# Kernel optimization log

Measured on AMD Instinct MI355X. Metric: run time of the kernel, lower is better.

Reference implementation:

```python
import jax, jax.numpy as jnp
import numpy as np

B, T, D_MODEL, NHEAD, D_HEAD = 8, 4096, 1024, 16, 64


def setup_inputs() -> dict:
    key = jax.random.key(0)
    ks = jax.random.split(key, 8)
    return {
        "inputs": jax.random.normal(ks[0], (B, T, D_MODEL), jnp.float32),
        "z0": jax.random.normal(ks[1], (NHEAD, D_HEAD), jnp.float32),
        "W_in": jax.random.normal(ks[2], (D_MODEL, D_MODEL), jnp.float32) / np.sqrt(D_MODEL),
        "b_in": jax.random.normal(ks[3], (D_MODEL,), jnp.float32) * 0.01,
        "W_out": jax.random.normal(ks[4], (D_MODEL, D_MODEL), jnp.float32) / np.sqrt(D_MODEL),
        "b_out": jax.random.normal(ks[5], (D_MODEL,), jnp.float32) * 0.01,
        "smoothing_logit": jax.random.normal(ks[6], (NHEAD, 1), jnp.float32),
        "v0": jax.random.normal(ks[7], (1, 1, NHEAD, D_HEAD), jnp.float32),
    }


def reference(inputs, z0, W_in, b_in, W_out, b_out, smoothing_logit, v0):
    b, t, d = inputs.shape
    nhead, d_head = z0.shape
    # in projection -> (b, t, h, d_head)
    values = (inputs @ W_in + b_in).reshape(b, t, nhead, d_head)
    # prepend learned z0, then temporal differencing -> (b, t, h, d_head)
    z0_b = jnp.broadcast_to(z0[None, None], (b, 1, nhead, d_head))
    values = jnp.concatenate([z0_b, values], axis=1)
    values = values[:, 1:] - values[:, :-1]
    # exponential smoothing recurrence: s_j = a*s_{j-1} + (1-a)*v_j, s_{-1} = v0
    alpha = jax.nn.sigmoid(smoothing_logit)           # (h, 1)
    a = alpha[None]                                   # (1, h, 1) broadcast over batch
    s0 = jnp.broadcast_to(v0[0, 0][None], (b, nhead, d_head))

    def step(s, v):                                   # v: (b, h, d_head)
        s = a * s + (1.0 - a) * v
        return s, s

    _, es_out = jax.lax.scan(step, s0, jnp.swapaxes(values, 0, 1))  # (t, b, h, d)
    es_out = jnp.swapaxes(es_out, 0, 1)               # (b, t, h, d_head)
    # prepend v0 -> length t+1
    v0_b = jnp.broadcast_to(v0, (b, 1, nhead, d_head))
    out = jnp.concatenate([v0_b, es_out], axis=1)     # (b, t+1, h, d_head)
    out = out.reshape(b, t + 1, nhead * d_head)
    return out @ W_out + b_out                        # (b, t+1, d_model)
```

## Files before the change

kernel.cpp:

```cpp
#include <hip/hip_runtime.h>
#include <hip/hip_bf16.h>
#include <stdint.h>

#define DEV static __device__ __forceinline__

typedef __attribute__((ext_vector_type(8))) short bf16x8;
typedef __attribute__((ext_vector_type(4))) float f32x4;
typedef unsigned int u32;

static constexpr int T = 4096;
static constexpr int BATCH = 8;
static constexpr int DM = 1024;
static constexpr int M1 = BATCH * T;
static constexpr int M2 = BATCH * (T + 1);
static constexpr int M2P = 257 * 128;
static constexpr int NCH = 64;
static constexpr int CL = T / NCH;
static constexpr int NT = 16;

DEV unsigned short f2bf(float f) {
  union { float f; unsigned u; } v; v.f = f;
  unsigned u = v.u;
  return (unsigned short)((u + 0x7fffu + ((u >> 16) & 1u)) >> 16);
}
DEV float bf2f(unsigned short s) {
  union { unsigned u; float f; } v; v.u = ((unsigned)s) << 16;
  return v.f;
}

DEV void gl_lds16(const unsigned short* g, unsigned short* lds) {
  __builtin_amdgcn_global_load_lds(
      (const __attribute__((address_space(1))) u32*)g,
      (__attribute__((address_space(3))) u32*)lds,
      16, 0, 0);
}

__global__ void k_cvt_x(const float4* __restrict__ x, ushort4* __restrict__ o) {
  int i = blockIdx.x * 256 + threadIdx.x;
  float4 v = x[i];
  ushort4 r;
  r.x = f2bf(v.x); r.y = f2bf(v.y); r.z = f2bf(v.z); r.w = f2bf(v.w);
  o[i] = r;
}

__global__ void k_transpose(const float* __restrict__ w0, const float* __restrict__ w1,
                            unsigned short* __restrict__ t0, unsigned short* __restrict__ t1) {
  __shared__ float tile[32][33];
  const float* src = blockIdx.z ? w1 : w0;
  unsigned short* dst = blockIdx.z ? t1 : t0;
  int bx = blockIdx.x * 32;
  int by = blockIdx.y * 32;
  int tx = threadIdx.x & 31, ty = threadIdx.x >> 5;
#pragma unroll
  for (int r = 0; r < 32; r += 8)
    tile[ty + r][tx] = src[(by + ty + r) * DM + bx + tx];
  __syncthreads();
#pragma unroll
  for (int r = 0; r < 32; r += 8)
    dst[(bx + ty + r) * DM + by + tx] = f2bf(tile[tx][ty + r]);
}

template <int MODE>
__global__ __launch_bounds__(256, 2) void k_gemm(const unsigned short* __restrict__ A16,
                                                 const unsigned short* __restrict__ Bt16,
                                                 const float* __restrict__ bias,
                                                 unsigned short* __restrict__ outb,
                                                 float* __restrict__ outf, int Mvalid) {
  __shared__ unsigned short lds[2][2][128 * 64];

  const int tid = threadIdx.x;
  const int w = tid >> 6, l = tid & 63;
  const int wm = w >> 1, wn = w & 1;
  const int lo = l & 15, hi = l >> 4;

  const int nwg = gridDim.x, orig = blockIdx.x;
  const int cpx = nwg >> 3;
  const int wg = (orig & 7) * cpx + (orig >> 3);
  const int bm = wg >> 3, bn = wg & 7;
  const int blockM = bm * 128;
  const int blockN = bn * 128;

  f32x4 acc[4][4];
#pragma unroll
  for (int m = 0; m < 4; m++)
#pragma unroll
    for (int n = 0; n < 4; n++) acc[m][n] = (f32x4){0.f, 0.f, 0.f, 0.f};

  const int ssw = (l & 7) ^ ((l >> 3) & 7);
  const unsigned short* pA[4];
  const unsigned short* pB[4];
#pragma unroll
  for (int c = 0; c < 4; c++) {
    const int rp = w * 32 + c * 8 + (l >> 3);
    pA[c] = A16 + (size_t)(blockM + rp) * DM + ssw * 8;
    pB[c] = Bt16 + (size_t)(blockN + rp) * DM + ssw * 8;
  }

  auto stage = [&](int tt, int buf) {
#pragma unroll
    for (int c = 0; c < 4; c++) {
      gl_lds16(pA[c] + (size_t)tt * 64, &lds[buf][0][(w * 32 + c * 8) * 64]);
      gl_lds16(pB[c] + (size_t)tt * 64, &lds[buf][1][(w * 32 + c * 8) * 64]);
    }
  };

  stage(0, 0);
  __syncthreads();

  for (int t = 0; t < NT; ++t) {
    const int cur = t & 1;
    if (t + 1 < NT) stage(t + 1, cur ^ 1);

    const unsigned short* La = lds[cur][0];
    const unsigned short* Lb = lds[cur][1];
    bf16x8 aq[4][2], bq[4][2];
#pragma unroll
    for (int kh = 0; kh < 2; kh++) {
      const int g = kh * 4 + hi;
#pragma unroll
      for (int mf = 0; mf < 4; mf++) {
        const int r = wm * 64 + mf * 16 + lo;
        aq[mf][kh] = *(const bf16x8*)(La + r * 64 + (g ^ (r & 7)) * 8);
      }
#pragma unroll
      for (int nf = 0; nf < 4; nf++) {
        const int r = wn * 64 + nf * 16 + lo;
        bq[nf][kh] = *(const bf16x8*)(Lb + r * 64 + (g ^ (r & 7)) * 8);
      }
    }
#pragma unroll
    for (int kh = 0; kh < 2; kh++)
#pragma unroll
      for (int mf = 0; mf < 4; mf++)
#pragma unroll
        for (int nf = 0; nf < 4; nf++)
          acc[mf][nf] = __builtin_amdgcn_mfma_f32_16x16x32_bf16(
              bq[nf][kh], aq[mf][kh], acc[mf][nf], 0, 0, 0);

    __syncthreads();
  }

#pragma unroll
  for (int mf = 0; mf < 4; mf++) {
    const int row = blockM + wm * 64 + mf * 16 + lo;
    if (MODE == 1 && row >= Mvalid) continue;
#pragma unroll
    for (int nf = 0; nf < 4; nf++) {
      const int col = blockN + wn * 64 + nf * 16 + hi * 4;
      const float4 bv = *(const float4*)(bias + col);
      if (MODE == 0) {
        ushort4 o;
        o.x = f2bf(acc[mf][nf][0] + bv.x);
        o.y = f2bf(acc[mf][nf][1] + bv.y);
        o.z = f2bf(acc[mf][nf][2] + bv.z);
        o.w = f2bf(acc[mf][nf][3] + bv.w);
        *(ushort4*)(outb + (size_t)row * DM + col) = o;
      } else {
        float4 o;
        o.x = acc[mf][nf][0] + bv.x;
        o.y = acc[mf][nf][1] + bv.y;
        o.z = acc[mf][nf][2] + bv.z;
        o.w = acc[mf][nf][3] + bv.w;
        *(float4*)(outf + (size_t)row * DM + col) = o;
      }
    }
  }
}

__global__ void k_scan_partial(const unsigned short* __restrict__ proj,
                               const float* __restrict__ logit,
                               const float* __restrict__ z0,
                               float* __restrict__ chunkend) {
  int b = blockIdx.x >> 6, c = blockIdx.x & 63;
  int ch = threadIdx.x;
  float a = 1.f / (1.f + expf(-logit[ch >> 6]));
  int t0 = c * CL;
  const unsigned short* p = proj + (size_t)(b * T + t0) * DM + ch;
  float pprev = (t0 == 0) ? z0[ch] : bf2f(p[-DM]);
  float s = 0.f;
  for (int j = 0; j < CL; j++) {
    float pv = bf2f(p[(size_t)j * DM]);
    s = a * s + (1.f - a) * (pv - pprev);
    pprev = pv;
  }
  chunkend[(b * NCH + c) * DM + ch] = s;
}

__global__ void k_scan_combine(const float* __restrict__ chunkend,
                               const float* __restrict__ logit,
                               const float* __restrict__ v0,
                               float* __restrict__ enter) {
  int b = blockIdx.x;
  int ch = threadIdx.x;
  float a = 1.f / (1.f + expf(-logit[ch >> 6]));
  float a2 = a * a, a4 = a2 * a2, a8 = a4 * a4, a16 = a8 * a8, a32 = a16 * a16;
  float aL = a32 * a32;
  float e = v0[ch];
  enter[(b * NCH + 0) * DM + ch] = e;
  for (int c = 1; c < NCH; c++) {
    e = aL * e + chunkend[(b * NCH + c - 1) * DM + ch];
    enter[(b * NCH + c) * DM + ch] = e;
  }
}

__global__ void k_scan_final(const unsigned short* __restrict__ proj,
                             const float* __restrict__ logit,
                             const float* __restrict__ z0,
                             const float* __restrict__ v0,
                             const float* __restrict__ enter,
                             unsigned short* __restrict__ S) {
  int b = blockIdx.x >> 6, c = blockIdx.x & 63;
  int ch = threadIdx.x;
  float a = 1.f / (1.f + expf(-logit[ch >> 6]));
  int t0 = c * CL;
  const unsigned short* p = proj + (size_t)(b * T + t0) * DM + ch;
  unsigned short* so = S + (size_t)(b * (T + 1) + t0 + 1) * DM + ch;
  float pprev = (t0 == 0) ? z0[ch] : bf2f(p[-DM]);
  float s = enter[(b * NCH + c) * DM + ch];
  if (c == 0) S[(size_t)b * (T + 1) * DM + ch] = f2bf(v0[ch]);
  for (int j = 0; j < CL; j++) {
    float pv = bf2f(p[(size_t)j * DM]);
    s = a * s + (1.f - a) * (pv - pprev);
    pprev = pv;
    so[(size_t)j * DM] = f2bf(s);
  }
}

__global__ void k_pad(unsigned short* __restrict__ S) {
  int i = blockIdx.x * 256 + threadIdx.x;
  S[(size_t)M2 * DM + i] = 0;
}

extern "C" void kernel_launch(void* const* d_in, const int* in_sizes, int n_in,
                              void* d_out, int out_size, void* d_ws, size_t ws_size,
                              hipStream_t stream) {
  const float* inputs = (const float*)d_in[0];
  const float* z0     = (const float*)d_in[1];
  const float* W_in   = (const float*)d_in[2];
  const float* b_in   = (const float*)d_in[3];
  const float* W_out  = (const float*)d_in[4];
  const float* b_out  = (const float*)d_in[5];
  const float* slogit = (const float*)d_in[6];
  const float* v0     = (const float*)d_in[7];
  float* out = (float*)d_out;

  char* ws = (char*)d_ws;
  unsigned short* X16   = (unsigned short*)(ws);
  unsigned short* P16   = (unsigned short*)(ws + 67108864);
  unsigned short* S16   = (unsigned short*)(ws + 134217728);
  unsigned short* WTin  = (unsigned short*)(ws + 201588736);
  unsigned short* WTout = (unsigned short*)(ws + 203685888);
  float* chunkend       = (float*)(ws + 205783040);
  float* enter          = (float*)(ws + 207880192);

  k_cvt_x<<<32768, 256, 0, stream>>>((const float4*)inputs, (ushort4*)X16);
  k_transpose<<<dim3(32, 32, 2), 256, 0, stream>>>(W_in, W_out, WTin, WTout);
  k_gemm<0><<<dim3((M1 / 128) * 8), 256, 0, stream>>>(X16, WTin, b_in, P16, nullptr, M1);
  k_scan_partial<<<dim3(BATCH * NCH), 1024, 0, stream>>>(P16, slogit, z0, chunkend);
  k_scan_combine<<<dim3(BATCH), 1024, 0, stream>>>(chunkend, slogit, v0, enter);
  k_scan_final<<<dim3(BATCH * NCH), 1024, 0, stream>>>(P16, slogit, z0, v0, enter, S16);
  k_pad<<<dim3(480), 256, 0, stream>>>(S16);
  k_gemm<1><<<dim3((M2P / 128) * 8), 256, 0, stream>>>(S16, WTout, b_out, nullptr, out, M2);
}
```

Before: 278.9 us.

## Fuse fp32-to-bf16 input conversion into first GEMM A-tile loading

Removes the standalone conversion kernel. The first GEMM now reads the fp32 inputs directly into registers, packs them to bf16 and writes them into swizzled LDS after the MFMA work, prefetching one k-tile ahead. This avoids writing and re-reading a bf16 copy of the activations. The zero-padding kernel for the second GEMM's pad rows is also dropped, since those rows are masked on store. In exchange, GEMM0 moves twice the A bytes through vector registers rather than async global-to-LDS loads, which adds register pressure and may reduce latency hiding.

```diff
diff --git a/kernel.cpp b/kernel.cpp
--- a/kernel.cpp
+++ b/kernel.cpp
@@ -27,20 +27,20 @@
   union { unsigned u; float f; } v; v.u = ((unsigned)s) << 16;
   return v.f;
 }
+DEV bf16x8 pack8(float4 a, float4 b) {
+  bf16x8 r;
+  r[0] = (short)f2bf(a.x); r[1] = (short)f2bf(a.y);
+  r[2] = (short)f2bf(a.z); r[3] = (short)f2bf(a.w);
+  r[4] = (short)f2bf(b.x); r[5] = (short)f2bf(b.y);
+  r[6] = (short)f2bf(b.z); r[7] = (short)f2bf(b.w);
+  return r;
+}
 
 DEV void gl_lds16(const unsigned short* g, unsigned short* lds) {
   __builtin_amdgcn_global_load_lds(
       (const __attribute__((address_space(1))) u32*)g,
       (__attribute__((address_space(3))) u32*)lds,
       16, 0, 0);
-}
-
-__global__ void k_cvt_x(const float4* __restrict__ x, ushort4* __restrict__ o) {
-  int i = blockIdx.x * 256 + threadIdx.x;
-  float4 v = x[i];
-  ushort4 r;
-  r.x = f2bf(v.x); r.y = f2bf(v.y); r.z = f2bf(v.z); r.w = f2bf(v.w);
-  o[i] = r;
 }
 
 __global__ void k_transpose(const float* __restrict__ w0, const float* __restrict__ w1,
@@ -61,7 +61,7 @@
 }
 
 template <int MODE>
-__global__ __launch_bounds__(256, 2) void k_gemm(const unsigned short* __restrict__ A16,
+__global__ __launch_bounds__(256, 2) void k_gemm(const void* __restrict__ Asrc,
                                                  const unsigned short* __restrict__ Bt16,
                                                  const float* __restrict__ bias,
                                                  unsigned short* __restrict__ outb,
@@ -80,6 +80,9 @@
   const int blockM = bm * 128;
   const int blockN = bn * 128;
 
+  const float* A32 = (const float*)Asrc;
+  const unsigned short* A16 = (const unsigned short*)Asrc;
+
   f32x4 acc[4][4];
 #pragma unroll
   for (int m = 0; m < 4; m++)
@@ -87,29 +90,60 @@
     for (int n = 0; n < 4; n++) acc[m][n] = (f32x4){0.f, 0.f, 0.f, 0.f};
 
   const int ssw = (l & 7) ^ ((l >> 3) & 7);
-  const unsigned short* pA[4];
   const unsigned short* pB[4];
+  const unsigned short* pA16[4];
 #pragma unroll
   for (int c = 0; c < 4; c++) {
     const int rp = w * 32 + c * 8 + (l >> 3);
-    pA[c] = A16 + (size_t)(blockM + rp) * DM + ssw * 8;
     pB[c] = Bt16 + (size_t)(blockN + rp) * DM + ssw * 8;
-  }
-
-  auto stage = [&](int tt, int buf) {
-#pragma unroll
-    for (int c = 0; c < 4; c++) {
-      gl_lds16(pA[c] + (size_t)tt * 64, &lds[buf][0][(w * 32 + c * 8) * 64]);
+    if (MODE == 1) pA16[c] = A16 + (size_t)(blockM + rp) * DM + ssw * 8;
+  }
+  auto stageB = [&](int tt, int buf) {
+#pragma unroll
+    for (int c = 0; c < 4; c++)
       gl_lds16(pB[c] + (size_t)tt * 64, &lds[buf][1][(w * 32 + c * 8) * 64]);
-    }
-  };
-
-  stage(0, 0);
+  };
+  auto stageA16 = [&](int tt, int buf) {
+#pragma unroll
+    for (int c = 0; c < 4; c++)
+      gl_lds16(pA16[c] + (size_t)tt * 64, &lds[buf][0][(w * 32 + c * 8) * 64]);
+  };
+
+  const int arow = tid >> 1;
+  const int akh = tid & 1;
+  const float* pA32 = A32 + (size_t)(blockM + arow) * DM + akh * 32;
+  float4 av[8];
+  auto loadA32 = [&](int tt) {
+#pragma unroll
+    for (int i = 0; i < 8; i++)
+      av[i] = *(const float4*)(pA32 + (size_t)tt * 64 + i * 4);
+  };
+  auto writeA32 = [&](int buf) {
+#pragma unroll
+    for (int s2 = 0; s2 < 4; s2++) {
+      const int s = akh * 4 + s2;
+      const int phys = s ^ (arow & 7);
+      *(bf16x8*)&lds[buf][0][arow * 64 + phys * 8] = pack8(av[s2 * 2], av[s2 * 2 + 1]);
+    }
+  };
+
+  if (MODE == 0) {
+    loadA32(0);
+    writeA32(0);
+  } else {
+    stageA16(0, 0);
+  }
+  stageB(0, 0);
   __syncthreads();
 
   for (int t = 0; t < NT; ++t) {
     const int cur = t & 1;
-    if (t + 1 < NT) stage(t + 1, cur ^ 1);
+    const bool hasN = (t + 1 < NT);
+    if (hasN) {
+      if (MODE == 0) loadA32(t + 1);
+      else           stageA16(t + 1, cur ^ 1);
+      stageB(t + 1, cur ^ 1);
+    }
 
     const unsigned short* La = lds[cur][0];
     const unsigned short* Lb = lds[cur][1];
@@ -136,6 +170,8 @@
         for (int nf = 0; nf < 4; nf++)
           acc[mf][nf] = __builtin_amdgcn_mfma_f32_16x16x32_bf16(
               bq[nf][kh], aq[mf][kh], acc[mf][nf], 0, 0, 0);
+
+    if (MODE == 0 && hasN) writeA32(cur ^ 1);
 
     __syncthreads();
   }
@@ -226,11 +262,6 @@
   }
 }
 
-__global__ void k_pad(unsigned short* __restrict__ S) {
-  int i = blockIdx.x * 256 + threadIdx.x;
-  S[(size_t)M2 * DM + i] = 0;
-}
-
 extern "C" void kernel_launch(void* const* d_in, const int* in_sizes, int n_in,
                               void* d_out, int out_size, void* d_ws, size_t ws_size,
                               hipStream_t stream) {
@@ -245,20 +276,17 @@
   float* out = (float*)d_out;
 
   char* ws = (char*)d_ws;
-  unsigned short* X16   = (unsigned short*)(ws);
-  unsigned short* P16   = (unsigned short*)(ws + 67108864);
-  unsigned short* S16   = (unsigned short*)(ws + 134217728);
-  unsigned short* WTin  = (unsigned short*)(ws + 201588736);
-  unsigned short* WTout = (unsigned short*)(ws + 203685888);
-  float* chunkend       = (float*)(ws + 205783040);
-  float* enter          = (float*)(ws + 207880192);
-
-  k_cvt_x<<<32768, 256, 0, stream>>>((const float4*)inputs, (ushort4*)X16);
+  unsigned short* P16   = (unsigned short*)(ws);
+  unsigned short* S16   = (unsigned short*)(ws + 67108864);
+  unsigned short* WTin  = (unsigned short*)(ws + 134479872);
+  unsigned short* WTout = (unsigned short*)(ws + 136577024);
+  float* chunkend       = (float*)(ws + 138674176);
+  float* enter          = (float*)(ws + 140771328);
+
   k_transpose<<<dim3(32, 32, 2), 256, 0, stream>>>(W_in, W_out, WTin, WTout);
-  k_gemm<0><<<dim3((M1 / 128) * 8), 256, 0, stream>>>(X16, WTin, b_in, P16, nullptr, M1);
+  k_gemm<0><<<dim3((M1 / 128) * 8), 256, 0, stream>>>(inputs, WTin, b_in, P16, nullptr, M1);
   k_scan_partial<<<dim3(BATCH * NCH), 1024, 0, stream>>>(P16, slogit, z0, chunkend);
   k_scan_combine<<<dim3(BATCH), 1024, 0, stream>>>(chunkend, slogit, v0, enter);
   k_scan_final<<<dim3(BATCH * NCH), 1024, 0, stream>>>(P16, slogit, z0, v0, enter, S16);
-  k_pad<<<dim3(480), 256, 0, stream>>>(S16);
   k_gemm<1><<<dim3((M2P / 128) * 8), 256, 0, stream>>>(S16, WTout, b_out, nullptr, out, M2);
 }
```

Result: slower. 349.9 us (+25.4%).

## Retile GEMM to 256x128 blocks with 8 waves and K-step 32

Applied to the files above, without the earlier changes.

Both bf16 GEMMs now use 256x128 output tiles computed by 512-thread (8-wave) workgroups, with a K tile of 32 instead of 64 and a new LDS swizzle. LDS use per block drops to 48KB, and launch bounds now allow more resident waves. The separate padding kernel is removed, since rows past the valid range are skipped at store time. The aim is more A-tile reuse per B load and better latency hiding, at the cost of twice as many K iterations and barriers.

```diff
diff --git a/kernel.cpp b/kernel.cpp
--- a/kernel.cpp
+++ b/kernel.cpp
@@ -13,10 +13,10 @@
 static constexpr int DM = 1024;
 static constexpr int M1 = BATCH * T;
 static constexpr int M2 = BATCH * (T + 1);
-static constexpr int M2P = 257 * 128;
+static constexpr int M2P = 129 * 256;
 static constexpr int NCH = 64;
 static constexpr int CL = T / NCH;
-static constexpr int NT = 16;
+static constexpr int NT = 32;
 
 DEV unsigned short f2bf(float f) {
   union { float f; unsigned u; } v; v.f = f;
@@ -61,12 +61,12 @@
 }
 
 template <int MODE>
-__global__ __launch_bounds__(256, 2) void k_gemm(const unsigned short* __restrict__ A16,
+__global__ __launch_bounds__(512, 4) void k_gemm(const unsigned short* __restrict__ A16,
                                                  const unsigned short* __restrict__ Bt16,
                                                  const float* __restrict__ bias,
                                                  unsigned short* __restrict__ outb,
                                                  float* __restrict__ outf, int Mvalid) {
-  __shared__ unsigned short lds[2][2][128 * 64];
+  __shared__ unsigned short lds[2][12288];
 
   const int tid = threadIdx.x;
   const int w = tid >> 6, l = tid & 63;
@@ -77,7 +77,7 @@
   const int cpx = nwg >> 3;
   const int wg = (orig & 7) * cpx + (orig >> 3);
   const int bm = wg >> 3, bn = wg & 7;
-  const int blockM = bm * 128;
+  const int blockM = bm * 256;
   const int blockN = bn * 128;
 
   f32x4 acc[4][4];
@@ -86,22 +86,19 @@
 #pragma unroll
     for (int n = 0; n < 4; n++) acc[m][n] = (f32x4){0.f, 0.f, 0.f, 0.f};
 
-  const int ssw = (l & 7) ^ ((l >> 3) & 7);
-  const unsigned short* pA[4];
-  const unsigned short* pB[4];
-#pragma unroll
-  for (int c = 0; c < 4; c++) {
-    const int rp = w * 32 + c * 8 + (l >> 3);
-    pA[c] = A16 + (size_t)(blockM + rp) * DM + ssw * 8;
-    pB[c] = Bt16 + (size_t)(blockN + rp) * DM + ssw * 8;
-  }
+  const int sg = (l & 3) ^ ((l >> 3) & 3);
+  const unsigned short* pA[2];
+#pragma unroll
+  for (int c = 0; c < 2; c++)
+    pA[c] = A16 + (size_t)(blockM + w * 32 + c * 16 + (l >> 2)) * DM + sg * 8;
+  const unsigned short* pB =
+      Bt16 + (size_t)(blockN + w * 16 + (l >> 2)) * DM + sg * 8;
 
   auto stage = [&](int tt, int buf) {
 #pragma unroll
-    for (int c = 0; c < 4; c++) {
-      gl_lds16(pA[c] + (size_t)tt * 64, &lds[buf][0][(w * 32 + c * 8) * 64]);
-      gl_lds16(pB[c] + (size_t)tt * 64, &lds[buf][1][(w * 32 + c * 8) * 64]);
-    }
+    for (int c = 0; c < 2; c++)
+      gl_lds16(pA[c] + (size_t)tt * 32, &lds[buf][(w * 32 + c * 16) * 32]);
+    gl_lds16(pB + (size_t)tt * 32, &lds[buf][8192 + (w * 16) * 32]);
   };
 
   stage(0, 0);
@@ -111,31 +108,23 @@
     const int cur = t & 1;
     if (t + 1 < NT) stage(t + 1, cur ^ 1);
 
-    const unsigned short* La = lds[cur][0];
-    const unsigned short* Lb = lds[cur][1];
-    bf16x8 aq[4][2], bq[4][2];
-#pragma unroll
-    for (int kh = 0; kh < 2; kh++) {
-      const int g = kh * 4 + hi;
-#pragma unroll
-      for (int mf = 0; mf < 4; mf++) {
-        const int r = wm * 64 + mf * 16 + lo;
-        aq[mf][kh] = *(const bf16x8*)(La + r * 64 + (g ^ (r & 7)) * 8);
-      }
-#pragma unroll
-      for (int nf = 0; nf < 4; nf++) {
-        const int r = wn * 64 + nf * 16 + lo;
-        bq[nf][kh] = *(const bf16x8*)(Lb + r * 64 + (g ^ (r & 7)) * 8);
-      }
+    bf16x8 aq[4], bq[4];
+#pragma unroll
+    for (int mf = 0; mf < 4; mf++) {
+      const int r = wm * 64 + mf * 16 + lo;
+      aq[mf] = *(const bf16x8*)(&lds[cur][r * 32 + (hi ^ ((r >> 1) & 3)) * 8]);
     }
 #pragma unroll
-    for (int kh = 0; kh < 2; kh++)
-#pragma unroll
-      for (int mf = 0; mf < 4; mf++)
-#pragma unroll
-        for (int nf = 0; nf < 4; nf++)
-          acc[mf][nf] = __builtin_amdgcn_mfma_f32_16x16x32_bf16(
-              bq[nf][kh], aq[mf][kh], acc[mf][nf], 0, 0, 0);
+    for (int nf = 0; nf < 4; nf++) {
+      const int r = wn * 64 + nf * 16 + lo;
+      bq[nf] = *(const bf16x8*)(&lds[cur][8192 + r * 32 + (hi ^ ((r >> 1) & 3)) * 8]);
+    }
+#pragma unroll
+    for (int mf = 0; mf < 4; mf++)
+#pragma unroll
+      for (int nf = 0; nf < 4; nf++)
+        acc[mf][nf] = __builtin_amdgcn_mfma_f32_16x16x32_bf16(
+            bq[nf], aq[mf], acc[mf][nf], 0, 0, 0);
 
     __syncthreads();
   }
@@ -226,11 +215,6 @@
   }
 }
 
-__global__ void k_pad(unsigned short* __restrict__ S) {
-  int i = blockIdx.x * 256 + threadIdx.x;
-  S[(size_t)M2 * DM + i] = 0;
-}
-
 extern "C" void kernel_launch(void* const* d_in, const int* in_sizes, int n_in,
                               void* d_out, int out_size, void* d_ws, size_t ws_size,
                               hipStream_t stream) {
@@ -248,17 +232,16 @@
   unsigned short* X16   = (unsigned short*)(ws);
   unsigned short* P16   = (unsigned short*)(ws + 67108864);
   unsigned short* S16   = (unsigned short*)(ws + 134217728);
-  unsigned short* WTin  = (unsigned short*)(ws + 201588736);
-  unsigned short* WTout = (unsigned short*)(ws + 203685888);
-  float* chunkend       = (float*)(ws + 205783040);
-  float* enter          = (float*)(ws + 207880192);
+  unsigned short* WTin  = (unsigned short*)(ws + 201850880);
+  unsigned short* WTout = (unsigned short*)(ws + 203948032);
+  float* chunkend       = (float*)(ws + 206045184);
+  float* enter          = (float*)(ws + 208142336);
 
   k_cvt_x<<<32768, 256, 0, stream>>>((const float4*)inputs, (ushort4*)X16);
   k_transpose<<<dim3(32, 32, 2), 256, 0, stream>>>(W_in, W_out, WTin, WTout);
-  k_gemm<0><<<dim3((M1 / 128) * 8), 256, 0, stream>>>(X16, WTin, b_in, P16, nullptr, M1);
+  k_gemm<0><<<dim3((M1 / 256) * 8), 512, 0, stream>>>(X16, WTin, b_in, P16, nullptr, M1);
   k_scan_partial<<<dim3(BATCH * NCH), 1024, 0, stream>>>(P16, slogit, z0, chunkend);
   k_scan_combine<<<dim3(BATCH), 1024, 0, stream>>>(chunkend, slogit, v0, enter);
   k_scan_final<<<dim3(BATCH * NCH), 1024, 0, stream>>>(P16, slogit, z0, v0, enter, S16);
-  k_pad<<<dim3(480), 256, 0, stream>>>(S16);
-  k_gemm<1><<<dim3((M2P / 128) * 8), 256, 0, stream>>>(S16, WTout, b_out, nullptr, out, M2);
-}
+  k_gemm<1><<<dim3((M2P / 256) * 8), 512, 0, stream>>>(S16, WTout, b_out, nullptr, out, M2);
+}
```

Result: no change. 276.3 us (-0.9%).
